# Kernel tuning notes

Measured on AMD Instinct MI355X. Metric: run time of the kernel, lower is better.

The kernel has to match this reference:

```python
import jax, jax.numpy as jnp
import numpy as np

INF = 1.0e12
B, L, D, H = 8, 128, 512, 8
DV = D // H

def _xavier(key, shape, fan_in, fan_out):
    a = float(np.sqrt(6.0 / (fan_in + fan_out)))
    return jax.random.uniform(key, shape, jnp.float32, -a, a)

def setup_inputs() -> dict:
    key = jax.random.key(0)
    ks = jax.random.split(key, 12)
    inp = jax.random.normal(ks[0], (B, L, D), jnp.float32)
    relation_inp = jax.random.normal(ks[1], (B, L, L, D), jnp.float32)
    mask = jnp.zeros((B, L, L), dtype=bool)  # no padding masked
    adj_mask = jax.random.randint(ks[2], (B, H, L, L), 0, 2).astype(jnp.int32)
    idx = jnp.arange(L)
    adj_mask = adj_mask.at[:, :, idx, idx].set(1)  # ensure non-empty neighborhoods
    rel_pos_mat = jnp.zeros((B, L, L), jnp.int32)
    deprel_mat = jnp.zeros((B, L, L), jnp.int32)
    deparc_mat = jnp.zeros((B, L, L), jnp.int32)
    W_value = _xavier(ks[3], (D, H * DV), D, H * DV)
    W_relation = _xavier(ks[4], (D, H * DV), D, H * DV)
    # weight vectors have torch shape (1,1,1,H,DV); xavier fan over last 2 dims
    w_src = _xavier(ks[5], (H, DV), H, DV)
    w_tgt = _xavier(ks[6], (H, DV), H, DV)
    w_rel = _xavier(ks[7], (H, DV), H, DV)
    W_final = _xavier(ks[8], (2 * D, D), 2 * D, D)
    b_final = jnp.zeros((D,), jnp.float32)
    return {"inp": inp, "relation_inp": relation_inp, "mask": mask,
            "adj_mask": adj_mask, "rel_pos_mat": rel_pos_mat,
            "deprel_mat": deprel_mat, "deparc_mat": deparc_mat,
            "W_value": W_value, "W_relation": W_relation,
            "w_src": w_src, "w_tgt": w_tgt, "w_rel": w_rel,
            "W_final": W_final, "b_final": b_final}

def _leaky(x):
    return jnp.where(x >= 0, x, 0.2 * x)

def reference(inp, relation_inp, mask, adj_mask, rel_pos_mat, deprel_mat,
              deparc_mat, W_value, W_relation, w_src, w_tgt, w_rel,
              W_final, b_final):
    b, l, d = inp.shape
    h, dv = w_src.shape
    # value: [B,H,L,DV]
    value = (inp @ W_value).reshape(b, l, h, dv).transpose(0, 2, 1, 3)
    # additive GAT scores without materializing [B,L,L,H,DV] src/tgt tensors
    e_src = jnp.einsum('bhld,hd->bhl', value, w_src)  # source index j
    e_tgt = jnp.einsum('bhld,hd->bhl', value, w_tgt)  # target index i
    scores_value = _leaky(e_tgt[:, :, :, None] + e_src[:, :, None, :])  # [B,H,L,L]
    # relation projection: [B,L,L,H,DV]
    relation = (relation_inp @ W_relation).reshape(b, l, l, h, dv)
    scores_relation = _leaky(jnp.einsum('bijhd,hd->bhij', relation, w_rel))
    # masks
    pad = mask[:, None]                       # [B,1,L,L] True = masked
    noadj = adj_mask == 0                     # [B,H,L,L]
    bad = pad | noadj
    scores_value = jnp.where(bad, -INF, scores_value)
    scores_relation = jnp.where(bad, -INF, scores_relation)
    attn_value = jax.nn.softmax(scores_value, axis=-1)
    attn_relation = jax.nn.softmax(scores_relation, axis=-1)
    # normalized: multiply by 1/adj (0 where no edge since adj in {0,1}), L1 renorm
    adjf = adj_mask.astype(attn_value.dtype)
    def renorm(a):
        a = a * adjf
        s = jnp.sum(jnp.abs(a), axis=-1, keepdims=True)
        return a / jnp.maximum(s, 1e-12)
    attn_value = renorm(attn_value)
    attn_relation = renorm(attn_relation)
    # zero masked / non-adjacent entries
    attn_value = jnp.where(bad, 0.0, attn_value)
    attn_relation = jnp.where(bad, 0.0, attn_relation)
    out_v = jnp.einsum('bhij,bhjd->bhid', attn_value, value)
    out_r = jnp.einsum('bhij,bhjd->bhid', attn_relation, value)
    out_v = out_v.transpose(0, 2, 1, 3).reshape(b, l, h * dv)
    out_r = out_r.transpose(0, 2, 1, 3).reshape(b, l, h * dv)
    final = jnp.concatenate([out_v, out_r], axis=-1) @ W_final + b_final
    final = final + inp
    return final, attn_value, attn_relation
```

## Files before the change

### kernel.cpp

```cpp
#include <hip/hip_runtime.h>

#define B_ 8
#define L_ 128
#define D_ 512
#define H_ 8

__device__ __forceinline__ float leaky(float v) { return fmaxf(v, 0.2f * v); }

__global__ __launch_bounds__(256) void k_wreff(const float* __restrict__ Wrel,
                                               const float* __restrict__ wrel,
                                               float* __restrict__ wr_eff) {
    int t = blockIdx.x * 256 + threadIdx.x;
    int k = t >> 3, h = t & 7;
    const float4* a = (const float4*)(Wrel + k * 512 + h * 64);
    const float4* b = (const float4*)(wrel + h * 64);
    float acc = 0.f;
#pragma unroll
    for (int q = 0; q < 16; q++) {
        float4 av = a[q], bv = b[q];
        acc += av.x * bv.x + av.y * bv.y + av.z * bv.z + av.w * bv.w;
    }
    wr_eff[k * 8 + h] = acc;
}

__global__ __launch_bounds__(256) void k_srel_value(
        const float* __restrict__ rel, const float* __restrict__ wr_eff,
        const float* __restrict__ inp, const float* __restrict__ Wv,
        const float* __restrict__ wsrc, const float* __restrict__ wtgt,
        float* __restrict__ s_rel, float* __restrict__ value_t,
        float* __restrict__ e_src, float* __restrict__ e_tgt) {
    __shared__ float xs[4][512];
    const int t = threadIdx.x;

    if (blockIdx.x < 2048) {
        const int lane = t & 63;
        const int wave = (blockIdx.x * 256 + t) >> 6;

        float wrl[64];
        {
            const float4* wp = (const float4*)(wr_eff + lane * 64);
#pragma unroll
            for (int q = 0; q < 16; q++) {
                float4 v = wp[q];
                wrl[q * 4 + 0] = v.x; wrl[q * 4 + 1] = v.y;
                wrl[q * 4 + 2] = v.z; wrl[q * 4 + 3] = v.w;
            }
        }

        const bool hi32 = (lane & 32) != 0;
        const bool hi16 = (lane & 16) != 0;
        const bool hi8  = (lane & 8) != 0;
        const int  hsel = (lane >> 3) & 7;

#pragma unroll 2
        for (int it = 0; it < 16; ++it) {
            int row = wave * 16 + it;
            const float4* rp = (const float4*)(rel + (size_t)row * 512 + lane * 8);
            float4 u0 = rp[0];
            float4 u1 = rp[1];
            float x[8];
            x[0] = u0.x; x[1] = u0.y; x[2] = u0.z; x[3] = u0.w;
            x[4] = u1.x; x[5] = u1.y; x[6] = u1.z; x[7] = u1.w;
            float acc[8] = {0.f,0.f,0.f,0.f,0.f,0.f,0.f,0.f};
#pragma unroll
            for (int kk = 0; kk < 8; kk++)
#pragma unroll
                for (int h = 0; h < 8; h++)
                    acc[h] = fmaf(x[kk], wrl[kk * 8 + h], acc[h]);

            float a4[4];
#pragma unroll
            for (int hh = 0; hh < 4; hh++) {
                float send = hi32 ? acc[hh] : acc[hh + 4];
                float recv = __shfl_xor(send, 32, 64);
                float own  = hi32 ? acc[hh + 4] : acc[hh];
                a4[hh] = own + recv;
            }
            float a2[2];
#pragma unroll
            for (int hh = 0; hh < 2; hh++) {
                float send = hi16 ? a4[hh] : a4[hh + 2];
                float recv = __shfl_xor(send, 16, 64);
                float own  = hi16 ? a4[hh + 2] : a4[hh];
                a2[hh] = own + recv;
            }
            float send = hi8 ? a2[0] : a2[1];
            float recv = __shfl_xor(send, 8, 64);
            float a1 = (hi8 ? a2[1] : a2[0]) + recv;
            a1 += __shfl_xor(a1, 4, 64);
            a1 += __shfl_xor(a1, 2, 64);
            a1 += __shfl_xor(a1, 1, 64);

            if ((lane & 7) == 0) {
                float v = leaky(a1);
                int b = row >> 14, rem = row & 16383;
                s_rel[(((size_t)(b * 8 + hsel)) << 14) + rem] = v;
            }
        }
        return;
    }

    const int row0 = (blockIdx.x - 2048) * 4;
    {
        int r = t >> 6, seg = t & 63;
        const float4* ip = (const float4*)(inp + (size_t)(row0 + r) * 512 + seg * 8);
        float4 a = ip[0], bq = ip[1];
        *(float4*)&xs[r][seg * 8]     = a;
        *(float4*)&xs[r][seg * 8 + 4] = bq;
    }
    __syncthreads();
    const int c0 = t * 2;
    float acc[4][2] = {};
    for (int k0 = 0; k0 < 512; k0 += 4) {
        float4 xr[4];
#pragma unroll
        for (int r = 0; r < 4; r++) xr[r] = *(const float4*)&xs[r][k0];
#define VSTEP(COMP, I)                                                          \
        {                                                                       \
            float2 wv = *(const float2*)(Wv + (size_t)(k0 + I) * 512 + c0);     \
            _Pragma("unroll")                                                   \
            for (int r = 0; r < 4; r++) {                                       \
                acc[r][0] = fmaf(xr[r].COMP, wv.x, acc[r][0]);                  \
                acc[r][1] = fmaf(xr[r].COMP, wv.y, acc[r][1]);                  \
            }                                                                   \
        }
        VSTEP(x, 0) VSTEP(y, 1) VSTEP(z, 2) VSTEP(w, 3)
#undef VSTEP
    }
    const int h = t >> 5;
    const int d0 = c0 & 63;
    const int b = row0 >> 7, l0 = row0 & 127;
    {
        float4 v0 = make_float4(acc[0][0], acc[1][0], acc[2][0], acc[3][0]);
        float4 v1 = make_float4(acc[0][1], acc[1][1], acc[2][1], acc[3][1]);
        *(float4*)&value_t[((size_t)((b * 8 + h) * 64 + d0)) * 128 + l0] = v0;
        *(float4*)&value_t[((size_t)((b * 8 + h) * 64 + d0 + 1)) * 128 + l0] = v1;
    }
    float ws0 = wsrc[c0], ws1 = wsrc[c0 + 1];
    float wt0 = wtgt[c0], wt1 = wtgt[c0 + 1];
    float es[4], et[4];
#pragma unroll
    for (int r = 0; r < 4; r++) {
        es[r] = acc[r][0] * ws0 + acc[r][1] * ws1;
        et[r] = acc[r][0] * wt0 + acc[r][1] * wt1;
    }
#pragma unroll
    for (int off = 16; off >= 1; off >>= 1)
#pragma unroll
        for (int r = 0; r < 4; r++) {
            es[r] += __shfl_xor(es[r], off, 64);
            et[r] += __shfl_xor(et[r], off, 64);
        }
    if ((t & 31) == 0) {
#pragma unroll
        for (int r = 0; r < 4; r++) {
            e_src[(b * 8 + h) * 128 + l0 + r] = es[r];
            e_tgt[(b * 8 + h) * 128 + l0 + r] = et[r];
        }
    }
}

__global__ __launch_bounds__(512) void k_attn_final(
        const float* s_rel, const float* __restrict__ value_t,
        const float* __restrict__ e_src, const float* __restrict__ e_tgt,
        const int* __restrict__ adj, const unsigned char* __restrict__ mask,
        const float* __restrict__ Wf, const float* __restrict__ bias,
        const float* __restrict__ inp,
        float* __restrict__ out_av, float* out_ar, float* __restrict__ outf) {
    __shared__ float xls[4][1024];
    __shared__ float ltmp[2048];
    const int t = threadIdx.x;
    const int lane = t & 63;
    const int w = t >> 6;
    const int r = w >> 1;
    const int hh = w & 1;
    const int b = blockIdx.x >> 5;
    const int iq = blockIdx.x & 31;
    const int i = iq * 4 + r;
    const int j0 = lane, j1 = lane + 64;
    float* lav = &ltmp[w * 256];
    float* lar = lav + 128;

    const unsigned char m0 = mask[(size_t)(b * 128 + i) * 128 + j0];
    const unsigned char m1 = mask[(size_t)(b * 128 + i) * 128 + j1];

    for (int h8 = 0; h8 < 4; h8++) {
        const int h = hh * 4 + h8;
        const int bh = b * 8 + h;
        const size_t rowbase = ((size_t)bh * 128 + i) * 128;
        const float etg = e_tgt[bh * 128 + i];

        float sv0 = leaky(etg + e_src[bh * 128 + j0]);
        float sv1 = leaky(etg + e_src[bh * 128 + j1]);
        float sr0 = s_rel[rowbase + j0];
        float sr1 = s_rel[rowbase + j1];
        int a0 = adj[rowbase + j0], a1 = adj[rowbase + j1];
        bool bad0 = m0 || (a0 == 0);
        bool bad1 = m1 || (a1 == 0);
        if (bad0) { sv0 = -1e30f; sr0 = -1e30f; }
        if (bad1) { sv1 = -1e30f; sr1 = -1e30f; }

        float mv = fmaxf(sv0, sv1), mr = fmaxf(sr0, sr1);
#pragma unroll
        for (int off = 32; off >= 1; off >>= 1) {
            mv = fmaxf(mv, __shfl_xor(mv, off, 64));
            mr = fmaxf(mr, __shfl_xor(mr, off, 64));
        }
        float pv0 = bad0 ? 0.f : __expf(sv0 - mv);
        float pv1 = bad1 ? 0.f : __expf(sv1 - mv);
        float pr0 = bad0 ? 0.f : __expf(sr0 - mr);
        float pr1 = bad1 ? 0.f : __expf(sr1 - mr);
        float sumv = pv0 + pv1, sumr = pr0 + pr1;
#pragma unroll
        for (int off = 32; off >= 1; off >>= 1) {
            sumv += __shfl_xor(sumv, off, 64);
            sumr += __shfl_xor(sumr, off, 64);
        }
        float iv = 1.f / fmaxf(sumv, 1e-12f);
        float ir = 1.f / fmaxf(sumr, 1e-12f);
        float av0 = pv0 * iv, av1 = pv1 * iv;
        float ar0 = pr0 * ir, ar1 = pr1 * ir;

        out_av[rowbase + j0] = av0;
        out_av[rowbase + j1] = av1;
        out_ar[rowbase + j0] = ar0;
        out_ar[rowbase + j1] = ar1;

        lav[j0] = av0; lav[j1] = av1;
        lar[j0] = ar0; lar[j1] = ar1;

        const float4* vrow = (const float4*)(value_t + ((size_t)bh * 64 + lane) * 128);
        float accv = 0.f, accr = 0.f;
#pragma unroll 8
        for (int jb = 0; jb < 32; jb++) {
            float4 v4 = vrow[jb];
            float4 a4 = *(const float4*)&lav[jb * 4];
            float4 r4 = *(const float4*)&lar[jb * 4];
            accv = fmaf(a4.x, v4.x, accv); accv = fmaf(a4.y, v4.y, accv);
            accv = fmaf(a4.z, v4.z, accv); accv = fmaf(a4.w, v4.w, accv);
            accr = fmaf(r4.x, v4.x, accr); accr = fmaf(r4.y, v4.y, accr);
            accr = fmaf(r4.z, v4.z, accr); accr = fmaf(r4.w, v4.w, accr);
        }
        xls[r][h * 64 + lane] = accv;
        xls[r][512 + h * 64 + lane] = accr;
    }
    __syncthreads();

    const int g  = t >> 8;
    const int tt = t & 255;
    const int c0 = tt * 2;
    const int kb = g * 512;
    float acc[4][2] = {};
    for (int k0 = 0; k0 < 512; k0 += 4) {
        float4 xr[4];
#pragma unroll
        for (int rr = 0; rr < 4; rr++) xr[rr] = *(const float4*)&xls[rr][kb + k0];
#define FSTEP(COMP, I)                                                          \
        {                                                                       \
            float2 wv = *(const float2*)(Wf + (size_t)(kb + k0 + I) * 512 + c0);\
            _Pragma("unroll")                                                   \
            for (int rr = 0; rr < 4; rr++) {                                    \
                acc[rr][0] = fmaf(xr[rr].COMP, wv.x, acc[rr][0]);               \
                acc[rr][1] = fmaf(xr[rr].COMP, wv.y, acc[rr][1]);               \
            }                                                                   \
        }
        FSTEP(x, 0) FSTEP(y, 1) FSTEP(z, 2) FSTEP(w, 3)
#undef FSTEP
    }
    if (g == 1) {
#pragma unroll
        for (int rr = 0; rr < 4; rr++)
            *(float2*)&ltmp[rr * 512 + c0] = make_float2(acc[rr][0], acc[rr][1]);
    }
    __syncthreads();
    if (g == 0) {
        const int row0 = blockIdx.x * 4;
        float b0 = bias[c0], b1 = bias[c0 + 1];
#pragma unroll
        for (int rr = 0; rr < 4; rr++) {
            size_t ro = (size_t)(row0 + rr) * 512;
            float2 p   = *(const float2*)&ltmp[rr * 512 + c0];
            float2 ivl = *(const float2*)(inp + ro + c0);
            float v0 = acc[rr][0] + p.x + b0 + ivl.x;
            float v1 = acc[rr][1] + p.y + b1 + ivl.y;
            *(float2*)&outf[ro + c0] = make_float2(v0, v1);
        }
    }
}

extern "C" void kernel_launch(void* const* d_in, const int* in_sizes, int n_in,
                              void* d_out, int out_size, void* d_ws, size_t ws_size,
                              hipStream_t stream) {
    const float* inp  = (const float*)d_in[0];
    const float* rel  = (const float*)d_in[1];
    const unsigned char* mask = (const unsigned char*)d_in[2];
    const int*   adj  = (const int*)d_in[3];
    const float* Wv   = (const float*)d_in[7];
    const float* Wr   = (const float*)d_in[8];
    const float* wsrc = (const float*)d_in[9];
    const float* wtgt = (const float*)d_in[10];
    const float* wrel = (const float*)d_in[11];
    const float* Wf   = (const float*)d_in[12];
    const float* bfin = (const float*)d_in[13];

    float* outf   = (float*)d_out;
    float* out_av = outf + (size_t)B_ * L_ * D_;
    float* out_ar = out_av + (size_t)B_ * H_ * L_ * L_;

    char* ws = (char*)d_ws;
    float* wr_eff  = (float*)(ws);
    float* value_t = (float*)(ws + 16384);
    float* e_src   = (float*)(ws + 2113536);
    float* e_tgt   = (float*)(ws + 2146304);

    k_wreff<<<16, 256, 0, stream>>>(Wr, wrel, wr_eff);
    k_srel_value<<<2304, 256, 0, stream>>>(rel, wr_eff, inp, Wv, wsrc, wtgt,
                                           out_ar, value_t, e_src, e_tgt);
    k_attn_final<<<256, 512, 0, stream>>>(out_ar, value_t, e_src, e_tgt, adj, mask,
                                          Wf, bfin, inp, out_av, out_ar, outf);
}
```

Baseline: 495.2 us.

## Split attention and final projection into separate kernels with higher parallelism

The fused attention-plus-projection kernel becomes two kernels. One runs per (batch, head, 4-row) block, stages value rows in LDS with an XOR swizzle, and writes the concatenated attention outputs to a workspace buffer. The other is a tiled GEMM over 32x64 output tiles that adds bias and the residual. The goal is more concurrent blocks and less serial per-block work on Wf, at the cost of an extra global round trip for the intermediate and one more kernel launch.

```diff
diff --git a/kernel.cpp b/kernel.cpp
--- a/kernel.cpp
+++ b/kernel.cpp
@@ -160,131 +160,142 @@
     }
 }
 
-__global__ __launch_bounds__(512) void k_attn_final(
+__global__ __launch_bounds__(256) void k_attn(
         const float* s_rel, const float* __restrict__ value_t,
         const float* __restrict__ e_src, const float* __restrict__ e_tgt,
         const int* __restrict__ adj, const unsigned char* __restrict__ mask,
-        const float* __restrict__ Wf, const float* __restrict__ bias,
-        const float* __restrict__ inp,
-        float* __restrict__ out_av, float* out_ar, float* __restrict__ outf) {
-    __shared__ float xls[4][1024];
-    __shared__ float ltmp[2048];
+        float* __restrict__ out_av, float* out_ar, float* __restrict__ X) {
+    __shared__ float4 vs4[64][32];
+    __shared__ float ltmp[1024];
     const int t = threadIdx.x;
     const int lane = t & 63;
     const int w = t >> 6;
-    const int r = w >> 1;
-    const int hh = w & 1;
-    const int b = blockIdx.x >> 5;
-    const int iq = blockIdx.x & 31;
-    const int i = iq * 4 + r;
+    const int h = blockIdx.x & 7;
+    const int iq = (blockIdx.x >> 3) & 31;
+    const int b = blockIdx.x >> 8;
+    const int bh = b * 8 + h;
+
+#pragma unroll
+    for (int q = 0; q < 8; q++) {
+        int f = q * 256 + t;
+        int d = f >> 5, c4 = f & 31;
+        vs4[d][c4 ^ (d & 7)] =
+            *(const float4*)(value_t + ((size_t)bh * 64 + d) * 128 + c4 * 4);
+    }
+    __syncthreads();
+
+    const int i = iq * 4 + w;
     const int j0 = lane, j1 = lane + 64;
+    const size_t rowbase = ((size_t)bh * 128 + i) * 128;
+
+    const unsigned char m0 = mask[(size_t)(b * 128 + i) * 128 + j0];
+    const unsigned char m1 = mask[(size_t)(b * 128 + i) * 128 + j1];
+    const float etg = e_tgt[bh * 128 + i];
+
+    float sv0 = leaky(etg + e_src[bh * 128 + j0]);
+    float sv1 = leaky(etg + e_src[bh * 128 + j1]);
+    float sr0 = s_rel[rowbase + j0];
+    float sr1 = s_rel[rowbase + j1];
+    int a0 = adj[rowbase + j0], a1 = adj[rowbase + j1];
+    bool bad0 = m0 || (a0 == 0);
+    bool bad1 = m1 || (a1 == 0);
+    if (bad0) { sv0 = -1e30f; sr0 = -1e30f; }
+    if (bad1) { sv1 = -1e30f; sr1 = -1e30f; }
+
+    float mv = fmaxf(sv0, sv1), mr = fmaxf(sr0, sr1);
+#pragma unroll
+    for (int off = 32; off >= 1; off >>= 1) {
+        mv = fmaxf(mv, __shfl_xor(mv, off, 64));
+        mr = fmaxf(mr, __shfl_xor(mr, off, 64));
+    }
+    float pv0 = bad0 ? 0.f : __expf(sv0 - mv);
+    float pv1 = bad1 ? 0.f : __expf(sv1 - mv);
+    float pr0 = bad0 ? 0.f : __expf(sr0 - mr);
+    float pr1 = bad1 ? 0.f : __expf(sr1 - mr);
+    float sumv = pv0 + pv1, sumr = pr0 + pr1;
+#pragma unroll
+    for (int off = 32; off >= 1; off >>= 1) {
+        sumv += __shfl_xor(sumv, off, 64);
+        sumr += __shfl_xor(sumr, off, 64);
+    }
+    float iv = 1.f / fmaxf(sumv, 1e-12f);
+    float ir = 1.f / fmaxf(sumr, 1e-12f);
+    float av0 = pv0 * iv, av1 = pv1 * iv;
+    float ar0 = pr0 * ir, ar1 = pr1 * ir;
+
+    out_av[rowbase + j0] = av0;
+    out_av[rowbase + j1] = av1;
+    out_ar[rowbase + j0] = ar0;
+    out_ar[rowbase + j1] = ar1;
+
     float* lav = &ltmp[w * 256];
     float* lar = lav + 128;
-
-    const unsigned char m0 = mask[(size_t)(b * 128 + i) * 128 + j0];
-    const unsigned char m1 = mask[(size_t)(b * 128 + i) * 128 + j1];
-
-    for (int h8 = 0; h8 < 4; h8++) {
-        const int h = hh * 4 + h8;
-        const int bh = b * 8 + h;
-        const size_t rowbase = ((size_t)bh * 128 + i) * 128;
-        const float etg = e_tgt[bh * 128 + i];
-
-        float sv0 = leaky(etg + e_src[bh * 128 + j0]);
-        float sv1 = leaky(etg + e_src[bh * 128 + j1]);
-        float sr0 = s_rel[rowbase + j0];
-        float sr1 = s_rel[rowbase + j1];
-        int a0 = adj[rowbase + j0], a1 = adj[rowbase + j1];
-        bool bad0 = m0 || (a0 == 0);
-        bool bad1 = m1 || (a1 == 0);
-        if (bad0) { sv0 = -1e30f; sr0 = -1e30f; }
-        if (bad1) { sv1 = -1e30f; sr1 = -1e30f; }
-
-        float mv = fmaxf(sv0, sv1), mr = fmaxf(sr0, sr1);
-#pragma unroll
-        for (int off = 32; off >= 1; off >>= 1) {
-            mv = fmaxf(mv, __shfl_xor(mv, off, 64));
-            mr = fmaxf(mr, __shfl_xor(mr, off, 64));
-        }
-        float pv0 = bad0 ? 0.f : __expf(sv0 - mv);
-        float pv1 = bad1 ? 0.f : __expf(sv1 - mv);
-        float pr0 = bad0 ? 0.f : __expf(sr0 - mr);
-        float pr1 = bad1 ? 0.f : __expf(sr1 - mr);
-        float sumv = pv0 + pv1, sumr = pr0 + pr1;
-#pragma unroll
-        for (int off = 32; off >= 1; off >>= 1) {
-            sumv += __shfl_xor(sumv, off, 64);
-            sumr += __shfl_xor(sumr, off, 64);
-        }
-        float iv = 1.f / fmaxf(sumv, 1e-12f);
-        float ir = 1.f / fmaxf(sumr, 1e-12f);
-        float av0 = pv0 * iv, av1 = pv1 * iv;
-        float ar0 = pr0 * ir, ar1 = pr1 * ir;
-
-        out_av[rowbase + j0] = av0;
-        out_av[rowbase + j1] = av1;
-        out_ar[rowbase + j0] = ar0;
-        out_ar[rowbase + j1] = ar1;
-
-        lav[j0] = av0; lav[j1] = av1;
-        lar[j0] = ar0; lar[j1] = ar1;
-
-        const float4* vrow = (const float4*)(value_t + ((size_t)bh * 64 + lane) * 128);
-        float accv = 0.f, accr = 0.f;
+    lav[j0] = av0; lav[j1] = av1;
+    lar[j0] = ar0; lar[j1] = ar1;
+
+    float accv = 0.f, accr = 0.f;
 #pragma unroll 8
-        for (int jb = 0; jb < 32; jb++) {
-            float4 v4 = vrow[jb];
-            float4 a4 = *(const float4*)&lav[jb * 4];
-            float4 r4 = *(const float4*)&lar[jb * 4];
-            accv = fmaf(a4.x, v4.x, accv); accv = fmaf(a4.y, v4.y, accv);
-            accv = fmaf(a4.z, v4.z, accv); accv = fmaf(a4.w, v4.w, accv);
-            accr = fmaf(r4.x, v4.x, accr); accr = fmaf(r4.y, v4.y, accr);
-            accr = fmaf(r4.z, v4.z, accr); accr = fmaf(r4.w, v4.w, accr);
-        }
-        xls[r][h * 64 + lane] = accv;
-        xls[r][512 + h * 64 + lane] = accr;
-    }
-    __syncthreads();
-
-    const int g  = t >> 8;
-    const int tt = t & 255;
-    const int c0 = tt * 2;
-    const int kb = g * 512;
+    for (int jb = 0; jb < 32; jb++) {
+        float4 v4 = vs4[lane][jb ^ (lane & 7)];
+        float4 a4 = *(const float4*)&lav[jb * 4];
+        float4 r4 = *(const float4*)&lar[jb * 4];
+        accv = fmaf(a4.x, v4.x, accv); accv = fmaf(a4.y, v4.y, accv);
+        accv = fmaf(a4.z, v4.z, accv); accv = fmaf(a4.w, v4.w, accv);
+        accr = fmaf(r4.x, v4.x, accr); accr = fmaf(r4.y, v4.y, accr);
+        accr = fmaf(r4.z, v4.z, accr); accr = fmaf(r4.w, v4.w, accr);
+    }
+    const int row = b * 128 + i;
+    X[(size_t)row * 1024 + h * 64 + lane] = accv;
+    X[(size_t)row * 1024 + 512 + h * 64 + lane] = accr;
+}
+
+__global__ __launch_bounds__(256) void k_final_gemm(
+        const float* __restrict__ X, const float* __restrict__ Wf,
+        const float* __restrict__ bias, const float* __restrict__ inp,
+        float* __restrict__ outf) {
+    __shared__ float xs[32][128];
+    const int t = threadIdx.x;
+    const int R0 = (blockIdx.x >> 3) * 32;
+    const int C0 = (blockIdx.x & 7) * 64;
+    const int rg = t >> 5;
+    const int c = C0 + (t & 31) * 2;
     float acc[4][2] = {};
-    for (int k0 = 0; k0 < 512; k0 += 4) {
-        float4 xr[4];
-#pragma unroll
-        for (int rr = 0; rr < 4; rr++) xr[rr] = *(const float4*)&xls[rr][kb + k0];
-#define FSTEP(COMP, I)                                                          \
-        {                                                                       \
-            float2 wv = *(const float2*)(Wf + (size_t)(kb + k0 + I) * 512 + c0);\
-            _Pragma("unroll")                                                   \
-            for (int rr = 0; rr < 4; rr++) {                                    \
-                acc[rr][0] = fmaf(xr[rr].COMP, wv.x, acc[rr][0]);               \
-                acc[rr][1] = fmaf(xr[rr].COMP, wv.y, acc[rr][1]);               \
-            }                                                                   \
-        }
-        FSTEP(x, 0) FSTEP(y, 1) FSTEP(z, 2) FSTEP(w, 3)
-#undef FSTEP
-    }
-    if (g == 1) {
-#pragma unroll
-        for (int rr = 0; rr < 4; rr++)
-            *(float2*)&ltmp[rr * 512 + c0] = make_float2(acc[rr][0], acc[rr][1]);
-    }
-    __syncthreads();
-    if (g == 0) {
-        const int row0 = blockIdx.x * 4;
-        float b0 = bias[c0], b1 = bias[c0 + 1];
-#pragma unroll
-        for (int rr = 0; rr < 4; rr++) {
-            size_t ro = (size_t)(row0 + rr) * 512;
-            float2 p   = *(const float2*)&ltmp[rr * 512 + c0];
-            float2 ivl = *(const float2*)(inp + ro + c0);
-            float v0 = acc[rr][0] + p.x + b0 + ivl.x;
-            float v1 = acc[rr][1] + p.y + b1 + ivl.y;
-            *(float2*)&outf[ro + c0] = make_float2(v0, v1);
-        }
+    for (int kc = 0; kc < 1024; kc += 128) {
+        __syncthreads();
+#pragma unroll
+        for (int q = 0; q < 4; q++) {
+            int f = q * 256 + t;
+            int row = f >> 5, c4 = f & 31;
+            *(float4*)&xs[row][c4 * 4] =
+                *(const float4*)(X + (size_t)(R0 + row) * 1024 + kc + c4 * 4);
+        }
+        __syncthreads();
+        for (int k0 = 0; k0 < 128; k0 += 4) {
+            float4 xr[4];
+#pragma unroll
+            for (int rr = 0; rr < 4; rr++)
+                xr[rr] = *(const float4*)&xs[rg * 4 + rr][k0];
+#define GSTEP(COMP, I)                                                          \
+            {                                                                   \
+                float2 wv = *(const float2*)(Wf + (size_t)(kc + k0 + I) * 512 + c); \
+                _Pragma("unroll")                                               \
+                for (int rr = 0; rr < 4; rr++) {                                \
+                    acc[rr][0] = fmaf(xr[rr].COMP, wv.x, acc[rr][0]);           \
+                    acc[rr][1] = fmaf(xr[rr].COMP, wv.y, acc[rr][1]);           \
+                }                                                               \
+            }
+            GSTEP(x, 0) GSTEP(y, 1) GSTEP(z, 2) GSTEP(w, 3)
+#undef GSTEP
+        }
+    }
+    float b0 = bias[c], b1 = bias[c + 1];
+#pragma unroll
+    for (int rr = 0; rr < 4; rr++) {
+        int row = R0 + rg * 4 + rr;
+        size_t ro = (size_t)row * 512 + c;
+        float2 ivl = *(const float2*)(inp + ro);
+        *(float2*)&outf[ro] = make_float2(acc[rr][0] + b0 + ivl.x,
+                                          acc[rr][1] + b1 + ivl.y);
     }
 }
 
@@ -312,10 +323,12 @@
     float* value_t = (float*)(ws + 16384);
     float* e_src   = (float*)(ws + 2113536);
     float* e_tgt   = (float*)(ws + 2146304);
+    float* Xbuf    = (float*)(ws + 2179072);
 
     k_wreff<<<16, 256, 0, stream>>>(Wr, wrel, wr_eff);
     k_srel_value<<<2304, 256, 0, stream>>>(rel, wr_eff, inp, Wv, wsrc, wtgt,
                                            out_ar, value_t, e_src, e_tgt);
-    k_attn_final<<<256, 512, 0, stream>>>(out_ar, value_t, e_src, e_tgt, adj, mask,
-                                          Wf, bfin, inp, out_av, out_ar, outf);
-}
+    k_attn<<<2048, 256, 0, stream>>>(out_ar, value_t, e_src, e_tgt, adj, mask,
+                                     out_av, out_ar, Xbuf);
+    k_final_gemm<<<256, 256, 0, stream>>>(Xbuf, Wf, bfin, inp, outf);
+}
```

New measurement: 524.0 us. 1.06x slower.
